# Optimization experiments

Measured on AMD Instinct MI355X. Metric: run time of the kernel, lower is better.

Reference implementation:

```python
import jax, jax.numpy as jnp
import numpy as np

K = 3          # kernel_size
G = 8          # groups
R = 4          # channel reduction ratio
D = 1          # dilation
M = D * (K - 1)
M2 = M // 2


def setup_inputs() -> dict:
    key = jax.random.key(0)
    ks = jax.random.split(key, 5)
    B, C, Hin, Win = 8, 128, 130, 130
    Cr = C // R
    x = jax.random.normal(ks[0], (B, C, Hin, Win), jnp.float32)
    W_reduce = jax.random.normal(ks[1], (Cr, C), jnp.float32) / np.float32(np.sqrt(C))
    b_reduce = jax.random.normal(ks[2], (Cr,), jnp.float32) * 0.01
    W_kern = jax.random.normal(ks[3], (G * K * K, Cr), jnp.float32) / np.float32(np.sqrt(Cr))
    b_kern = jax.random.normal(ks[4], (G * K * K,), jnp.float32) * 0.01
    return dict(x=x, W_reduce=W_reduce, b_reduce=b_reduce, W_kern=W_kern, b_kern=b_kern)


def reference(x, W_reduce, b_reduce, W_kern, b_kern):
    B, C, Hin, Win = x.shape
    H, W = Hin - M, Win - M            # stride=1, padding=0
    CG = C // G
    # unfold (im2col), torch ordering: channel outer, kernel-position inner
    patches = jnp.stack(
        [x[:, :, i * D:i * D + H, j * D:j * D + W] for i in range(K) for j in range(K)],
        axis=2,
    )                                   # [B, C, K2, H, W]
    patches = patches.reshape(B, G, CG, K * K, H, W)
    # center crop for kernel generation (pool is Identity since stride=1)
    xc = x[:, :, M2:Hin - M2, M2:Win - M2]            # [B, C, H, W]
    red = jnp.einsum('rc,bchw->brhw', W_reduce, xc) + b_reduce[None, :, None, None]
    kern = jnp.einsum('or,brhw->bohw', W_kern, red) + b_kern[None, :, None, None]
    kern = kern.reshape(B, G, K * K, H, W)
    # per-pixel dynamic kernel multiply-sum over K2
    out = jnp.einsum('bgkhw,bgckhw->bgchw', kern, patches)
    return out.reshape(B, C, H, W)
```

## Files before the change

kernel.cpp:

```cpp
#include <hip/hip_runtime.h>

namespace {
constexpr int HIN = 130, WIN = 130;
constexpr int HH = 128, WW = 128;
constexpr int C = 128, CR = 32, B = 8;
constexpr int CHW = HIN * WIN;

__global__ void transpose_wred(const float* __restrict__ Wred, float* __restrict__ WredT) {
    int idx = blockIdx.x * 256 + threadIdx.x;
    int r = idx >> 7;
    int c = idx & 127;
    WredT[c * CR + r] = Wred[r * C + c];
}

__device__ __forceinline__ void lgkm_barrier() {
    asm volatile("s_waitcnt lgkmcnt(0)\n\ts_barrier" ::: "memory");
    __builtin_amdgcn_sched_barrier(0);
}

__global__ __launch_bounds__(256, 4) void invol_direct(
    const float* __restrict__ x,
    const float* __restrict__ WredT,
    const float* __restrict__ bred,
    const float* __restrict__ Wkern,
    const float* __restrict__ bkern,
    float* __restrict__ out)
{
    __shared__ float red2[CR][128];

    const int t = threadIdx.x;
    const int p = t & 63;
    const int q = __builtin_amdgcn_readfirstlane(t >> 6);

    const int orig = blockIdx.x;
    const int blk  = (orig & 7) * 128 + (orig >> 3);
    const int b    = blk >> 7;
    const int h    = blk & (HH - 1);

    const float* xb = x + (size_t)b * C * CHW;

    const float* xc = xb + (size_t)(h + 1) * WIN + (2 * p + 1);
    float r0[8], r1[8];
#pragma unroll
    for (int r = 0; r < 8; ++r) { r0[r] = bred[q * 8 + r]; r1[r] = r0[r]; }

#pragma unroll
    for (int cb = 0; cb < 4; ++cb) {
        float xv0[32], xv1[32];
#pragma unroll
        for (int cc = 0; cc < 32; ++cc) {
            const float* cp = xc + (size_t)(cb * 32 + cc) * CHW;
            xv0[cc] = cp[0];
            xv1[cc] = cp[1];
        }
#pragma unroll
        for (int cc = 0; cc < 32; ++cc) {
#pragma unroll
            for (int r = 0; r < 8; ++r) {
                float wgt = WredT[(cb * 32 + cc) * CR + q * 8 + r];
                r0[r] = fmaf(wgt, xv0[cc], r0[r]);
                r1[r] = fmaf(wgt, xv1[cc], r1[r]);
            }
        }
    }
#pragma unroll
    for (int r = 0; r < 8; ++r)
        *(float2*)&red2[q * 8 + r][2 * p] = make_float2(r0[r], r1[r]);

    lgkm_barrier();

    float k0[18], k1[18];
#pragma unroll
    for (int k = 0; k < 18; ++k) { k0[k] = bkern[18 * q + k]; k1[k] = k0[k]; }
#pragma unroll
    for (int r = 0; r < CR; ++r) {
        float2 rv = *(const float2*)&red2[r][2 * p];
#pragma unroll
        for (int k = 0; k < 18; ++k) {
            float wgt = Wkern[(18 * q + k) * CR + r];
            k0[k] = fmaf(wgt, rv.x, k0[k]);
            k1[k] = fmaf(wgt, rv.y, k1[k]);
        }
    }

    const float* xrow = xb + (size_t)h * WIN + 2 * p;
    float* op = out + (((size_t)(b * C + 32 * q)) * HH + h) * WW + 2 * p;

#pragma unroll
    for (int half = 0; half < 2; ++half) {
        float kh0[9], kh1[9];
#pragma unroll
        for (int k = 0; k < 9; ++k) { kh0[k] = k0[9 * half + k]; kh1[k] = k1[9 * half + k]; }

#pragma unroll 2
        for (int cc = 0; cc < 16; ++cc) {
            const float* xp = xrow + (size_t)(32 * q + 16 * half + cc) * CHW;
            float2 ta[3], tb[3];
#pragma unroll
            for (int i = 0; i < 3; ++i) {
                ta[i] = *(const float2*)(xp + i * WIN);
                tb[i] = *(const float2*)(xp + i * WIN + 2);
            }
            float a0 = 0.f, a1 = 0.f;
#pragma unroll
            for (int i = 0; i < 3; ++i) {
                a0 = fmaf(kh0[3 * i + 0], ta[i].x, a0);
                a0 = fmaf(kh0[3 * i + 1], ta[i].y, a0);
                a0 = fmaf(kh0[3 * i + 2], tb[i].x, a0);
                a1 = fmaf(kh1[3 * i + 0], ta[i].y, a1);
                a1 = fmaf(kh1[3 * i + 1], tb[i].x, a1);
                a1 = fmaf(kh1[3 * i + 2], tb[i].y, a1);
            }
            *(float2*)(op + (size_t)(16 * half + cc) * HH * WW) = make_float2(a0, a1);
        }
    }
}
}

extern "C" void kernel_launch(void* const* d_in, const int* in_sizes, int n_in,
                              void* d_out, int out_size, void* d_ws, size_t ws_size,
                              hipStream_t stream) {
    const float* x     = (const float*)d_in[0];
    const float* Wred  = (const float*)d_in[1];
    const float* bred  = (const float*)d_in[2];
    const float* Wkern = (const float*)d_in[3];
    const float* bkern = (const float*)d_in[4];
    float* out   = (float*)d_out;
    float* WredT = (float*)d_ws;

    transpose_wred<<<16, 256, 0, stream>>>(Wred, WredT);

    invol_direct<<<1024, 256, 0, stream>>>(x, WredT, bred, Wkern, bkern, out);
}
```

Before: 58.59 us.

## Stage center-row channels in LDS cooperatively with register prefetch

Previously every wave loaded all 128 channels of the center row for its own reduction slice, so each block read the same data four times from global memory. Now the block loads the center row cooperatively into a 32-channel LDS tile, one element per thread per channel. The next 32-channel chunk is prefetched into registers while the current chunk is consumed. This cuts redundant global traffic in the kernel-generation phase, at the cost of extra LDS (16KB), additional barriers per chunk, and higher register pressure from the prefetch buffer.

```diff
diff --git a/kernel.cpp b/kernel.cpp
--- a/kernel.cpp
+++ b/kernel.cpp
@@ -26,6 +26,7 @@
     const float* __restrict__ bkern,
     float* __restrict__ out)
 {
+    __shared__ float cs[32][128];
     __shared__ float red2[CR][128];
 
     const int t = threadIdx.x;
@@ -39,30 +40,49 @@
 
     const float* xb = x + (size_t)b * C * CHW;
 
-    const float* xc = xb + (size_t)(h + 1) * WIN + (2 * p + 1);
+    const float* cbase = xb + (size_t)(h + 1) * WIN + 1;
+    const int ch_off = t >> 7;
+    const int col    = t & 127;
+
     float r0[8], r1[8];
 #pragma unroll
     for (int r = 0; r < 8; ++r) { r0[r] = bred[q * 8 + r]; r1[r] = r0[r]; }
 
+    float st[16];
 #pragma unroll
-    for (int cb = 0; cb < 4; ++cb) {
-        float xv0[32], xv1[32];
+    for (int j = 0; j < 16; ++j)
+        st[j] = cbase[(size_t)(2 * j + ch_off) * CHW + col];
 #pragma unroll
-        for (int cc = 0; cc < 32; ++cc) {
-            const float* cp = xc + (size_t)(cb * 32 + cc) * CHW;
-            xv0[cc] = cp[0];
-            xv1[cc] = cp[1];
+    for (int j = 0; j < 16; ++j)
+        cs[2 * j + ch_off][col] = st[j];
+    lgkm_barrier();
+
+#pragma unroll
+    for (int k = 0; k < 4; ++k) {
+        if (k < 3) {
+#pragma unroll
+            for (int j = 0; j < 16; ++j)
+                st[j] = cbase[(size_t)(32 * (k + 1) + 2 * j + ch_off) * CHW + col];
         }
 #pragma unroll
         for (int cc = 0; cc < 32; ++cc) {
+            float2 xv = *(const float2*)&cs[cc][2 * p];
 #pragma unroll
             for (int r = 0; r < 8; ++r) {
-                float wgt = WredT[(cb * 32 + cc) * CR + q * 8 + r];
-                r0[r] = fmaf(wgt, xv0[cc], r0[r]);
-                r1[r] = fmaf(wgt, xv1[cc], r1[r]);
+                float wgt = WredT[(32 * k + cc) * CR + q * 8 + r];
+                r0[r] = fmaf(wgt, xv.x, r0[r]);
+                r1[r] = fmaf(wgt, xv.y, r1[r]);
             }
         }
+        if (k < 3) {
+            lgkm_barrier();
+#pragma unroll
+            for (int j = 0; j < 16; ++j)
+                cs[2 * j + ch_off][col] = st[j];
+            lgkm_barrier();
+        }
     }
+
 #pragma unroll
     for (int r = 0; r < 8; ++r)
         *(float2*)&red2[q * 8 + r][2 * p] = make_float2(r0[r], r1[r]);
```

After: 62.05 us. 5.9% more time.

## Stage center-pixel channels through LDS with double-buffered async global_load_lds

Applied to the files above, without the earlier changes.

Moves the center-crop input loads for the channel reduction out of per-thread register loads and into LDS. Each wave asynchronously stages 8 channels with global_load_lds into one of two buffers, and all waves then read from shared memory. This removes the 4x redundant global loads across waves and overlaps loading the next 32-channel chunk with the FMA work on the current one. In exchange it doubles shared memory per block and adds barriers with hand-counted vmcnt waits, which are fragile if the load count changes.

```diff
diff --git a/kernel.cpp b/kernel.cpp
--- a/kernel.cpp
+++ b/kernel.cpp
@@ -1,4 +1,5 @@
 #include <hip/hip_runtime.h>
+#include <stdint.h>
 
 namespace {
 constexpr int HIN = 130, WIN = 130;
@@ -18,6 +19,23 @@
     __builtin_amdgcn_sched_barrier(0);
 }
 
+template<int N>
+__device__ __forceinline__ void vmcnt_barrier() {
+    asm volatile("s_waitcnt vmcnt(%0)\n\ts_barrier" :: "i"(N) : "memory");
+    __builtin_amdgcn_sched_barrier(0);
+}
+
+__device__ __forceinline__ void vm0lgkm_barrier() {
+    asm volatile("s_waitcnt vmcnt(0) lgkmcnt(0)\n\ts_barrier" ::: "memory");
+    __builtin_amdgcn_sched_barrier(0);
+}
+
+__device__ __forceinline__ void stage256(const float* g, float* l) {
+    __builtin_amdgcn_global_load_lds(
+        (const __attribute__((address_space(1))) uint32_t*)g,
+        (__attribute__((address_space(3))) uint32_t*)l, 4, 0, 0);
+}
+
 __global__ __launch_bounds__(256, 4) void invol_direct(
     const float* __restrict__ x,
     const float* __restrict__ WredT,
@@ -26,7 +44,10 @@
     const float* __restrict__ bkern,
     float* __restrict__ out)
 {
-    __shared__ float red2[CR][128];
+    __shared__ union SM {
+        float cs[2][32][128];
+        struct { float red2[32][128]; } r;
+    } sm;
 
     const int t = threadIdx.x;
     const int p = t & 63;
@@ -39,42 +60,63 @@
 
     const float* xb = x + (size_t)b * C * CHW;
 
-    const float* xc = xb + (size_t)(h + 1) * WIN + (2 * p + 1);
+    const float* cbase = xb + (size_t)(h + 1) * WIN + 1;
+
     float r0[8], r1[8];
 #pragma unroll
     for (int r = 0; r < 8; ++r) { r0[r] = bred[q * 8 + r]; r1[r] = r0[r]; }
 
-#pragma unroll
-    for (int cb = 0; cb < 4; ++cb) {
-        float xv0[32], xv1[32];
-#pragma unroll
-        for (int cc = 0; cc < 32; ++cc) {
-            const float* cp = xc + (size_t)(cb * 32 + cc) * CHW;
-            xv0[cc] = cp[0];
-            xv1[cc] = cp[1];
-        }
-#pragma unroll
-        for (int cc = 0; cc < 32; ++cc) {
-#pragma unroll
-            for (int r = 0; r < 8; ++r) {
-                float wgt = WredT[(cb * 32 + cc) * CR + q * 8 + r];
-                r0[r] = fmaf(wgt, xv0[cc], r0[r]);
-                r1[r] = fmaf(wgt, xv1[cc], r1[r]);
-            }
-        }
-    }
+#define ISSUE(k, bi) do { \
+    _Pragma("unroll") \
+    for (int j = 0; j < 8; ++j) { \
+        const float* g_ = cbase + (size_t)(32 * (k) + q * 8 + j) * CHW; \
+        stage256(g_ + p,      &sm.cs[bi][q * 8 + j][0]); \
+        stage256(g_ + 64 + p, &sm.cs[bi][q * 8 + j][64]); \
+    } \
+} while (0)
+
+#define CONSUME(k, bi) do { \
+    _Pragma("unroll") \
+    for (int cc = 0; cc < 32; ++cc) { \
+        float2 xv_ = *(const float2*)&sm.cs[bi][cc][2 * p]; \
+        _Pragma("unroll") \
+        for (int r = 0; r < 8; ++r) { \
+            float wgt_ = WredT[(32 * (k) + cc) * CR + q * 8 + r]; \
+            r0[r] = fmaf(wgt_, xv_.x, r0[r]); \
+            r1[r] = fmaf(wgt_, xv_.y, r1[r]); \
+        } \
+    } \
+} while (0)
+
+    ISSUE(0, 0); ISSUE(1, 1);
+    vmcnt_barrier<16>();
+    CONSUME(0, 0);
+    lgkm_barrier();
+    ISSUE(2, 0);
+    vmcnt_barrier<16>();
+    CONSUME(1, 1);
+    lgkm_barrier();
+    ISSUE(3, 1);
+    vmcnt_barrier<16>();
+    CONSUME(2, 0);
+    vm0lgkm_barrier();
+    CONSUME(3, 1);
+
 #pragma unroll
     for (int r = 0; r < 8; ++r)
-        *(float2*)&red2[q * 8 + r][2 * p] = make_float2(r0[r], r1[r]);
+        *(float2*)&sm.r.red2[q * 8 + r][2 * p] = make_float2(r0[r], r1[r]);
 
     lgkm_barrier();
+
+#undef ISSUE
+#undef CONSUME
 
     float k0[18], k1[18];
 #pragma unroll
     for (int k = 0; k < 18; ++k) { k0[k] = bkern[18 * q + k]; k1[k] = k0[k]; }
 #pragma unroll
     for (int r = 0; r < CR; ++r) {
-        float2 rv = *(const float2*)&red2[r][2 * p];
+        float2 rv = *(const float2*)&sm.r.red2[r][2 * p];
 #pragma unroll
         for (int k = 0; k < 18; ++k) {
             float wgt = Wkern[(18 * q + k) * CR + r];
```

New measurement: 61.83 us. +5.5%, slower.
